# Kernel optimization log

Hardware: AMD Instinct MI355X
Metric: run time of the kernel (lower is better)

The kernel has to match this reference:

```python
import jax, jax.numpy as jnp
import numpy as np

NUM_AGENTS = 64
IN_FEATURES = 512
OUT_FEATURES = 512
BATCH = 2048


def setup_inputs() -> dict:
    key = jax.random.key(0)
    k1, k2, k3, k4 = jax.random.split(key, 4)
    which_agents = jax.random.randint(k1, (BATCH,), 0, NUM_AGENTS, dtype=jnp.int64 if jax.config.jax_enable_x64 else jnp.int32)
    x = jax.random.normal(k2, (BATCH, IN_FEATURES), dtype=jnp.float32)
    # kaiming_uniform_(a=sqrt(5)) -> bound = sqrt(6 / ((1 + 5) * fan_in)) = 1/sqrt(fan_in)
    bound_w = 1.0 / np.sqrt(IN_FEATURES)
    weight = jax.random.uniform(k3, (NUM_AGENTS, OUT_FEATURES, IN_FEATURES), jnp.float32, -bound_w, bound_w)
    bound_b = 1.0 / np.sqrt(IN_FEATURES)
    bias = jax.random.uniform(k4, (NUM_AGENTS, OUT_FEATURES), jnp.float32, -bound_b, bound_b)
    return {"which_agents": which_agents, "input": x, "weight": weight, "bias": bias}


def reference(which_agents, input, weight, bias):
    # weight[which_agents]: [B, out, in]; batched matvec with input [B, in]
    w = weight[which_agents]          # [B, O, I]
    b = bias[which_agents]            # [B, O]
    return jnp.einsum('boi,bi->bo', w, input) + b
```

## Files before the change

kernel.cpp:

```cpp
#include <hip/hip_runtime.h>


constexpr int BATCH  = 2048;
constexpr int NAGENT = 64;
constexpr int IN_F   = 512;
constexpr int OUT_F  = 512;

constexpr int BN  = 128;
constexpr int MCH = 64;
constexpr int XS  = IN_F + 8;

typedef __attribute__((ext_vector_type(8))) short short8;
typedef __attribute__((ext_vector_type(4))) float f32x4;
typedef __attribute__((ext_vector_type(4))) unsigned int u32x4;

__device__ inline unsigned rnd_bf(float f) {
  unsigned u = __float_as_uint(f);
  return u + 0x7FFFu + ((u >> 16) & 1u);
}
__device__ inline unsigned pk_bf(float lo, float hi) {
  return (rnd_bf(lo) >> 16) | (rnd_bf(hi) & 0xFFFF0000u);
}

__global__ __launch_bounds__(1024, 4) void agent_linear_mfma2(
    const int*   __restrict__ which,
    const float* __restrict__ x,
    const float* __restrict__ weight,
    const float* __restrict__ bias,
    float*       __restrict__ out) {
  const int tid   = threadIdx.x;
  const int lane  = tid & 63;
  const int wid   = tid >> 6;
  const int w8    = wid & 7;
  const int kh    = wid >> 3;
  const int agent = blockIdx.y;
  const int obase = blockIdx.x * BN;

  __shared__ int rowlist_s[BATCH];
  __shared__ int wsum_s[16];
  __shared__ __align__(16) unsigned short Xs[MCH * XS];
  __shared__ float Rs[8][MCH][17];

  int2 v = ((const int2*)which)[tid];
  int lc = (v.x == agent) + (v.y == agent);
  int s = lc;
#pragma unroll
  for (int off = 1; off < 64; off <<= 1) {
    int t = __shfl_up(s, off);
    if (lane >= off) s += t;
  }
  if (lane == 63) wsum_s[wid] = s;
  __syncthreads();
  int base = 0, count = 0;
#pragma unroll
  for (int w = 0; w < 16; ++w) {
    int ws = wsum_s[w];
    if (w < wid) base += ws;
    count += ws;
  }
  {
    int pos = base + s - lc;
    if (v.x == agent) rowlist_s[pos++] = 2 * tid;
    if (v.y == agent) rowlist_s[pos]   = 2 * tid + 1;
  }

  const int nl = lane & 15;
  const int kq = lane >> 4;

  const float* wp = weight + ((size_t)(agent * OUT_F + obase + w8 * 16 + nl)) * IN_F
                  + kh * 256 + kq * 8;
  const float  bv = bias[agent * OUT_F + obase + w8 * 16 + nl];

  for (int m0 = 0; m0 < count; m0 += MCH) {
    const int mcount = min(MCH, count - m0);
    __syncthreads();

#pragma unroll
    for (int t = 0; t < 8; ++t) {
      int idx = t * 1024 + tid;
      int r   = idx >> 7;
      int c4  = idx & 127;
      uint2 w2 = {0u, 0u};
      if (r < mcount) {
        float4 xv = *(const float4*)(x + (size_t)rowlist_s[m0 + r] * IN_F + c4 * 4);
        w2.x = pk_bf(xv.x, xv.y);
        w2.y = pk_bf(xv.z, xv.w);
      }
      *(uint2*)&Xs[r * XS + c4 * 4] = w2;
    }
    __syncthreads();

    f32x4 acc[4] = {{0.f,0.f,0.f,0.f},{0.f,0.f,0.f,0.f},
                    {0.f,0.f,0.f,0.f},{0.f,0.f,0.f,0.f}};
    const int kbase = kh * 256;
    float4 pa[2], pb[2];
    pa[0] = *(const float4*)(wp);      pb[0] = *(const float4*)(wp + 4);
    pa[1] = *(const float4*)(wp + 32); pb[1] = *(const float4*)(wp + 36);
#pragma unroll
    for (int k = 0; k < 8; ++k) {
      float4 c0 = pa[k & 1], c1 = pb[k & 1];
      if (k + 2 < 8) {
        pa[k & 1] = *(const float4*)(wp + (k + 2) * 32);
        pb[k & 1] = *(const float4*)(wp + (k + 2) * 32 + 4);
      }
      u32x4 q;
      q[0] = pk_bf(c0.x, c0.y); q[1] = pk_bf(c0.z, c0.w);
      q[2] = pk_bf(c1.x, c1.y); q[3] = pk_bf(c1.z, c1.w);
      short8 bf = __builtin_bit_cast(short8, q);
#pragma unroll
      for (int i = 0; i < 4; ++i) {
        short8 af = *(const short8*)&Xs[(i * 16 + nl) * XS + kbase + k * 32 + kq * 8];
        acc[i] = __builtin_amdgcn_mfma_f32_16x16x32_bf16(af, bf, acc[i], 0, 0, 0);
      }
    }

    if (kh == 1) {
#pragma unroll
      for (int i = 0; i < 4; ++i)
#pragma unroll
        for (int r = 0; r < 4; ++r)
          Rs[w8][i * 16 + kq * 4 + r][nl] = acc[i][r];
    }
    __syncthreads();

    if (kh == 0) {
#pragma unroll
      for (int i = 0; i < 4; ++i) {
#pragma unroll
        for (int r = 0; r < 4; ++r) {
          int m = i * 16 + kq * 4 + r;
          if (m < mcount) {
            out[(size_t)rowlist_s[m0 + m] * OUT_F + obase + w8 * 16 + nl] =
                acc[i][r] + Rs[w8][m][nl] + bv;
          }
        }
      }
    }
  }
}

extern "C" void kernel_launch(void* const* d_in, const int* in_sizes, int n_in,
                              void* d_out, int out_size, void* d_ws, size_t ws_size,
                              hipStream_t stream) {
  const int*   which = (const int*)d_in[0];
  const float* x     = (const float*)d_in[1];
  const float* w     = (const float*)d_in[2];
  const float* b     = (const float*)d_in[3];
  float*       out   = (float*)d_out;

  dim3 grid(OUT_F / BN, NAGENT);
  agent_linear_mfma2<<<grid, dim3(1024), 0, stream>>>(which, x, w, b, out);
}
```

Measured before the change: 107.9 us.

## Shrink blocks to 256 threads with full-K per wave, dropping split-K reduction

Blocks shrink from 1024 to 256 threads, with 64 output columns per block, so the grid doubles to 8x64. Each wave now walks the full 512-wide K dimension instead of half of it, which removes the shared-memory split-K reduction buffer and its extra barrier. The scan over which_agents reads 8 entries per thread, and the weight prefetch depth grows to 4. In exchange, each block does more sequential work per wave and restages X twice as often across blocks, which adds redundant gather traffic for x.

Measured after the change: 115.0 us. 1.07x slower.

```diff
diff --git a/kernel.cpp b/kernel.cpp
--- a/kernel.cpp
+++ b/kernel.cpp
@@ -6,7 +6,7 @@
 constexpr int IN_F   = 512;
 constexpr int OUT_F  = 512;
 
-constexpr int BN  = 128;
+constexpr int BN  = 64;
 constexpr int MCH = 64;
 constexpr int XS  = IN_F + 8;
 
@@ -22,7 +22,7 @@
   return (rnd_bf(lo) >> 16) | (rnd_bf(hi) & 0xFFFF0000u);
 }
 
-__global__ __launch_bounds__(1024, 4) void agent_linear_mfma2(
+__global__ __launch_bounds__(256, 2) void agent_linear_v4(
     const int*   __restrict__ which,
     const float* __restrict__ x,
     const float* __restrict__ weight,
@@ -31,18 +31,24 @@
   const int tid   = threadIdx.x;
   const int lane  = tid & 63;
   const int wid   = tid >> 6;
-  const int w8    = wid & 7;
-  const int kh    = wid >> 3;
   const int agent = blockIdx.y;
   const int obase = blockIdx.x * BN;
 
+  __shared__ int wsum_s[4];
   __shared__ int rowlist_s[BATCH];
-  __shared__ int wsum_s[16];
   __shared__ __align__(16) unsigned short Xs[MCH * XS];
-  __shared__ float Rs[8][MCH][17];
 
-  int2 v = ((const int2*)which)[tid];
-  int lc = (v.x == agent) + (v.y == agent);
+  int vals[8];
+  {
+    const int4* w4 = (const int4*)which;
+    int4 v0 = w4[tid * 2];
+    int4 v1 = w4[tid * 2 + 1];
+    vals[0] = v0.x; vals[1] = v0.y; vals[2] = v0.z; vals[3] = v0.w;
+    vals[4] = v1.x; vals[5] = v1.y; vals[6] = v1.z; vals[7] = v1.w;
+  }
+  int lc = 0;
+#pragma unroll
+  for (int u = 0; u < 8; ++u) lc += (vals[u] == agent) ? 1 : 0;
   int s = lc;
 #pragma unroll
   for (int off = 1; off < 64; off <<= 1) {
@@ -53,55 +59,58 @@
   __syncthreads();
   int base = 0, count = 0;
 #pragma unroll
-  for (int w = 0; w < 16; ++w) {
+  for (int w = 0; w < 4; ++w) {
     int ws = wsum_s[w];
     if (w < wid) base += ws;
     count += ws;
   }
   {
     int pos = base + s - lc;
-    if (v.x == agent) rowlist_s[pos++] = 2 * tid;
-    if (v.y == agent) rowlist_s[pos]   = 2 * tid + 1;
+#pragma unroll
+    for (int u = 0; u < 8; ++u)
+      if (vals[u] == agent) rowlist_s[pos++] = tid * 8 + u;
   }
+  __syncthreads();
 
   const int nl = lane & 15;
   const int kq = lane >> 4;
 
-  const float* wp = weight + ((size_t)(agent * OUT_F + obase + w8 * 16 + nl)) * IN_F
-                  + kh * 256 + kq * 8;
-  const float  bv = bias[agent * OUT_F + obase + w8 * 16 + nl];
+  const float* wp = weight + ((size_t)(agent * OUT_F + obase + wid * 16 + nl)) * IN_F + kq * 8;
+  const float  bv = bias[agent * OUT_F + obase + wid * 16 + nl];
 
   for (int m0 = 0; m0 < count; m0 += MCH) {
     const int mcount = min(MCH, count - m0);
     __syncthreads();
 
-#pragma unroll
-    for (int t = 0; t < 8; ++t) {
-      int idx = t * 1024 + tid;
+#pragma unroll 4
+    for (int t = 0; t < 32; ++t) {
+      int idx = t * 256 + tid;
       int r   = idx >> 7;
       int c4  = idx & 127;
-      uint2 w2 = {0u, 0u};
       if (r < mcount) {
         float4 xv = *(const float4*)(x + (size_t)rowlist_s[m0 + r] * IN_F + c4 * 4);
+        uint2 w2;
         w2.x = pk_bf(xv.x, xv.y);
         w2.y = pk_bf(xv.z, xv.w);
+        *(uint2*)&Xs[r * XS + c4 * 4] = w2;
       }
-      *(uint2*)&Xs[r * XS + c4 * 4] = w2;
     }
     __syncthreads();
 
     f32x4 acc[4] = {{0.f,0.f,0.f,0.f},{0.f,0.f,0.f,0.f},
                     {0.f,0.f,0.f,0.f},{0.f,0.f,0.f,0.f}};
-    const int kbase = kh * 256;
-    float4 pa[2], pb[2];
-    pa[0] = *(const float4*)(wp);      pb[0] = *(const float4*)(wp + 4);
-    pa[1] = *(const float4*)(wp + 32); pb[1] = *(const float4*)(wp + 36);
+    float4 pa[4], pb[4];
 #pragma unroll
-    for (int k = 0; k < 8; ++k) {
-      float4 c0 = pa[k & 1], c1 = pb[k & 1];
-      if (k + 2 < 8) {
-        pa[k & 1] = *(const float4*)(wp + (k + 2) * 32);
-        pb[k & 1] = *(const float4*)(wp + (k + 2) * 32 + 4);
+    for (int p = 0; p < 4; ++p) {
+      pa[p] = *(const float4*)(wp + p * 32);
+      pb[p] = *(const float4*)(wp + p * 32 + 4);
+    }
+#pragma unroll
+    for (int k = 0; k < 16; ++k) {
+      float4 c0 = pa[k & 3], c1 = pb[k & 3];
+      if (k + 4 < 16) {
+        pa[k & 3] = *(const float4*)(wp + (k + 4) * 32);
+        pb[k & 3] = *(const float4*)(wp + (k + 4) * 32 + 4);
       }
       u32x4 q;
       q[0] = pk_bf(c0.x, c0.y); q[1] = pk_bf(c0.z, c0.w);
@@ -109,30 +118,19 @@
       short8 bf = __builtin_bit_cast(short8, q);
 #pragma unroll
       for (int i = 0; i < 4; ++i) {
-        short8 af = *(const short8*)&Xs[(i * 16 + nl) * XS + kbase + k * 32 + kq * 8];
+        short8 af = *(const short8*)&Xs[(i * 16 + nl) * XS + k * 32 + kq * 8];
         acc[i] = __builtin_amdgcn_mfma_f32_16x16x32_bf16(af, bf, acc[i], 0, 0, 0);
       }
     }
 
-    if (kh == 1) {
 #pragma unroll
-      for (int i = 0; i < 4; ++i)
+    for (int i = 0; i < 4; ++i) {
 #pragma unroll
-        for (int r = 0; r < 4; ++r)
-          Rs[w8][i * 16 + kq * 4 + r][nl] = acc[i][r];
-    }
-    __syncthreads();
-
-    if (kh == 0) {
-#pragma unroll
-      for (int i = 0; i < 4; ++i) {
-#pragma unroll
-        for (int r = 0; r < 4; ++r) {
-          int m = i * 16 + kq * 4 + r;
-          if (m < mcount) {
-            out[(size_t)rowlist_s[m0 + m] * OUT_F + obase + w8 * 16 + nl] =
-                acc[i][r] + Rs[w8][m][nl] + bv;
-          }
+      for (int r = 0; r < 4; ++r) {
+        int m = i * 16 + kq * 4 + r;
+        if (m < mcount) {
+          out[(size_t)rowlist_s[m0 + m] * OUT_F + obase + wid * 16 + nl] =
+              acc[i][r] + bv;
         }
       }
     }
@@ -149,5 +147,5 @@
   float*       out   = (float*)d_out;
 
   dim3 grid(OUT_F / BN, NAGENT);
-  agent_linear_mfma2<<<grid, dim3(1024), 0, stream>>>(which, x, w, b, out);
+  agent_linear_v4<<<grid, dim3(256), 0, stream>>>(which, x, w, b, out);
 }
```
